# Performance work log

Hardware: AMD Instinct MI355X
Metric: run time of the kernel (lower is better)

Reference implementation:

```python
import jax, jax.numpy as jnp
import numpy as np

CODEBOOK_SIZE = 8192
EMBED_DIM = 512
COMMITMENT_COST = 0.25
B, N = 16, 2048


def setup_inputs() -> dict:
    key = jax.random.key(0)
    kz, kc = jax.random.split(key)
    z = jax.random.normal(kz, (B, N, EMBED_DIM), dtype=jnp.float32)
    # torch init: uniform(-1/K, 1/K)
    scale = 1.0 / CODEBOOK_SIZE
    codebook = jax.random.uniform(kc, (CODEBOOK_SIZE, EMBED_DIM), dtype=jnp.float32,
                                  minval=-scale, maxval=scale)
    return {"z": z, "codebook": codebook}


def reference(z, codebook):
    Bd, Nd, D = z.shape
    flat_z = z.reshape(-1, D)  # (B*N, D)
    # squared L2 distances via expansion: ||z||^2 + ||e||^2 - 2 z.e
    distances = (jnp.sum(flat_z * flat_z, axis=1, keepdims=True)
                 + jnp.sum(codebook * codebook, axis=1)
                 - 2.0 * flat_z @ codebook.T)  # (B*N, K)
    indices = jnp.argmin(distances, axis=1)  # (B*N,)
    quantized = codebook[indices].reshape(Bd, Nd, D)
    # mse_loss default reduction='mean'
    codebook_loss = jnp.mean((jax.lax.stop_gradient(quantized) - z) ** 2)
    commitment_loss = jnp.mean((quantized - jax.lax.stop_gradient(z)) ** 2)
    vq_loss = codebook_loss + COMMITMENT_COST * commitment_loss
    # straight-through estimator
    quantized = z + jax.lax.stop_gradient(quantized - z)
    return quantized, indices.reshape(Bd, Nd), vq_loss
```

## Files before the change

### kernel.cpp

```cpp
#include <hip/hip_runtime.h>

#define M_ROWS 32768
#define DIM    512
#define KCB    8192
#define BM     128
#define BN     128
#define NSLAB  128

typedef int    i32x4  __attribute__((ext_vector_type(4)));
typedef unsigned long long u64;

#define AS1(p) ((const __attribute__((address_space(1))) void*)(p))
#define AS3(p) ((__attribute__((address_space(3))) void*)(p))

__global__ void __launch_bounds__(256)
vq_fragpack_i8(const float* __restrict__ x, unsigned char* __restrict__ dst,
               float scale, int nthr) {
    int u = blockIdx.x * 256 + threadIdx.x;
    if (u >= nthr) return;
    int l  = u & 63;
    int g  = (u >> 6) & 7;
    int s  = (u >> 9) & 7;
    int rb = u >> 12;
    int row = rb * 128 + g * 16 + (l & 15);
    int k   = s * 64 + (l >> 4) * 16;
    const float* src = x + (size_t)row * DIM + k;
    int dw[4];
    #pragma unroll
    for (int d4 = 0; d4 < 4; ++d4) {
        float4 v = *(const float4*)(src + d4 * 4);
        int b0 = __float2int_rn(v.x * scale);
        int b1 = __float2int_rn(v.y * scale);
        int b2 = __float2int_rn(v.z * scale);
        int b3 = __float2int_rn(v.w * scale);
        dw[d4] = (b0 & 255) | ((b1 & 255) << 8) | ((b2 & 255) << 16)
               | ((b3 & 255) << 24);
    }
    i32x4 o = { dw[0], dw[1], dw[2], dw[3] };
    *(i32x4*)(dst + (size_t)u * 16) = o;
}

__global__ void __launch_bounds__(256) vq_rownorm(const float* __restrict__ z,
                                                  float* __restrict__ A) {
    int row  = blockIdx.x * 4 + (threadIdx.x >> 6);
    int lane = threadIdx.x & 63;
    const float* zr = z + (size_t)row * DIM;
    float4 a = *(const float4*)(zr + lane * 4);
    float4 b = *(const float4*)(zr + 256 + lane * 4);
    float s = a.x*a.x + a.y*a.y + a.z*a.z + a.w*a.w
            + b.x*b.x + b.y*b.y + b.z*b.z + b.w*b.w;
    #pragma unroll
    for (int off = 32; off > 0; off >>= 1) s += __shfl_down(s, off, 64);
    if (lane == 0) A[row] = s;
}

__global__ void __launch_bounds__(256, 4)
vq_gemm(const unsigned char* __restrict__ zf, const unsigned char* __restrict__ ef,
        const float* __restrict__ Anorm, u64* __restrict__ cand) {
    extern __shared__ char lds[];
    const int tid  = threadIdx.x;
    const int lane = tid & 63;
    const int wid  = tid >> 6;
    const int wm   = wid >> 1;
    const int wn   = wid & 1;
    const int rb   = (int)blockIdx.x >> 6;
    const int cbk  = (int)blockIdx.x & 63;
    const char* zsrc = (const char*)zf + ((size_t)rb  << 16);
    const char* esrc = (const char*)ef + ((size_t)cbk << 16);

    i32x4 acc[4][4];
    #pragma unroll
    for (int m = 0; m < 4; ++m)
        #pragma unroll
        for (int n = 0; n < 4; ++n) acc[m][n] = (i32x4)0;

#define STAGE(t) do {                                                         \
    char* dst_ = lds + (((t) & 1) << 14);                                     \
    _Pragma("unroll")                                                         \
    for (int j = 0; j < 4; ++j) {                                             \
        int n2 = (wid << 2) | j;                    \
        const char* src_ = (n2 < 8)                                           \
            ? zsrc + (((t) << 13) + (n2 << 10)) + (lane << 4)                 \
            : esrc + (((t) << 13) + ((n2 - 8) << 10)) + (lane << 4);          \
        __builtin_amdgcn_global_load_lds(AS1(src_), AS3(dst_ + (n2 << 10)), 16, 0, 0); \
    }                                                                         \
} while (0)

#define COMPUTE(t) do {                                                       \
    const char* bufA_ = lds + (((t) & 1) << 14);                              \
    const char* bufB_ = bufA_ + 8192;                                         \
    i32x4 af[4];                                                              \
    _Pragma("unroll")                                                         \
    for (int m = 0; m < 4; ++m)                                               \
        af[m] = *(const i32x4*)(bufA_ + (((wm << 2) | m) << 10) + (lane << 4)); \
    i32x4 b0 = *(const i32x4*)(bufB_ + (((wn << 2) | 0) << 10) + (lane << 4)); \
    i32x4 b1 = *(const i32x4*)(bufB_ + (((wn << 2) | 1) << 10) + (lane << 4)); \
    __builtin_amdgcn_s_setprio(1);                                            \
    _Pragma("unroll")                                                         \
    for (int m = 0; m < 4; ++m) {                                             \
        acc[m][0] = __builtin_amdgcn_mfma_i32_16x16x64_i8(af[m], b0, acc[m][0], 0, 0, 0); \
        acc[m][1] = __builtin_amdgcn_mfma_i32_16x16x64_i8(af[m], b1, acc[m][1], 0, 0, 0); \
    }                                                                         \
    __builtin_amdgcn_s_setprio(0);                                            \
    i32x4 b2 = *(const i32x4*)(bufB_ + (((wn << 2) | 2) << 10) + (lane << 4)); \
    i32x4 b3 = *(const i32x4*)(bufB_ + (((wn << 2) | 3) << 10) + (lane << 4)); \
    __builtin_amdgcn_s_setprio(1);                                            \
    _Pragma("unroll")                                                         \
    for (int m = 0; m < 4; ++m) {                                             \
        acc[m][2] = __builtin_amdgcn_mfma_i32_16x16x64_i8(af[m], b2, acc[m][2], 0, 0, 0); \
        acc[m][3] = __builtin_amdgcn_mfma_i32_16x16x64_i8(af[m], b3, acc[m][3], 0, 0, 0); \
    }                                                                         \
    __builtin_amdgcn_s_setprio(0);                                            \
} while (0)

#define STEP2(t) do {                                                         \
    STAGE((t) + 1);                                                           \
    COMPUTE(t);                                                               \
    __syncthreads();                                                          \
} while (0)

    STAGE(0);
    __syncthreads();
    STEP2(0); STEP2(1); STEP2(2); STEP2(3); STEP2(4); STEP2(5); STEP2(6);
    COMPUTE(7);
    __syncthreads();

    const float INV = 2.0f / (16.0f * 8192.0f * 127.0f);
    float* As = (float*)lds;
    if (tid < BM) As[tid] = Anorm[rb * BM + tid];
    __syncthreads();

    const unsigned colbase = (unsigned)((cbk << 7) + (wn << 6) + (lane & 15));
    #pragma unroll
    for (int m = 0; m < 4; ++m) {
        #pragma unroll
        for (int rg = 0; rg < 4; ++rg) {
            int row_l = (wm << 6) + (m << 4) + ((lane >> 4) << 2) + rg;
            float Arow = As[row_l];
            unsigned abase = __float_as_uint(Arow) - 8192u;
            unsigned k1 = 0xFFFFFFFFu, k2 = 0xFFFFFFFFu;
            #pragma unroll
            for (int nj = 0; nj < 4; ++nj) {
                float t = (float)acc[m][nj][rg] * INV;
                float d = Arow - t;
                unsigned io = __float_as_uint(d) - abase;
                io = io > 65535u ? 65535u : io;
                unsigned key = io * 65536u + (colbase + (unsigned)(nj << 4));
                unsigned mx = key > k1 ? key : k1;
                k1 = key < k1 ? key : k1;
                k2 = mx < k2 ? mx : k2;
            }
            #pragma unroll
            for (int mk = 1; mk < 16; mk <<= 1) {
                unsigned o1 = (unsigned)__shfl_xor((int)k1, mk);
                unsigned o2 = (unsigned)__shfl_xor((int)k2, mk);
                unsigned lo = k1 < o1 ? k1 : o1;
                unsigned hi = k1 < o1 ? o1 : k1;
                unsigned so = k2 < o2 ? k2 : o2;
                k1 = lo;
                k2 = hi < so ? hi : so;
            }
            if ((lane & 15) == 0) {
                size_t base = (size_t)(rb * BM + row_l) * (2 * NSLAB)
                            + (size_t)(((cbk << 1) | wn) << 1);
                cand[base]     = ((u64)(abase + (k1 >> 16)) << 32) | (u64)(k1 & 0xFFFFu);
                cand[base + 1] = ((u64)(abase + (k2 >> 16)) << 32) | (u64)(k2 & 0xFFFFu);
            }
        }
    }
}

__global__ void __launch_bounds__(256)
vq_refine_gather(const float* __restrict__ z, const float* __restrict__ cb,
                 const float* __restrict__ Anorm, const u64* __restrict__ cand,
                 float* __restrict__ outQ, float* __restrict__ outIdx,
                 double* __restrict__ lossRow) {
    __shared__ float zs[4][DIM];
    __shared__ int   sc[4][128];
    int w = threadIdx.x >> 6, lane = threadIdx.x & 63;
    int row = blockIdx.x * 4 + w;

    const float* zr = z + (size_t)row * DIM;
    *(float4*)&zs[w][lane * 4]       = *(const float4*)(zr + lane * 4);
    *(float4*)&zs[w][256 + lane * 4] = *(const float4*)(zr + 256 + lane * 4);

    const u64* cr = cand + (size_t)row * (2 * NSLAB);
    u64 c[4];
    #pragma unroll
    for (int k = 0; k < 4; ++k) c[k] = cr[lane * 4 + k];
    u64 mn = c[0];
    #pragma unroll
    for (int k = 1; k < 4; ++k) if (c[k] < mn) mn = c[k];
    #pragma unroll
    for (int m = 32; m > 0; m >>= 1) { u64 o = __shfl_xor(mn, m); if (o < mn) mn = o; }
    float minD = __uint_as_float((unsigned)(mn >> 32));
    float thr = minD + 2e-3f;
    u64 below = ((u64)1 << lane) - 1;
    int base = 0;
    #pragma unroll
    for (int k = 0; k < 4; ++k) {
        bool sk = __uint_as_float((unsigned)(c[k] >> 32)) <= thr;
        u64 mk = __ballot(sk);
        if (sk) {
            int slot = base + __popcll(mk & below);
            if (slot < 128) sc[w][slot] = (int)(unsigned)c[k];
        }
        base += __popcll(mk);
    }
    int ns = base < 128 ? base : 128;
    __syncthreads();

    float Arow = Anorm[row];
    float4 zv0 = *(const float4*)&zs[w][lane * 8];
    float4 zv1 = *(const float4*)&zs[w][lane * 8 + 4];
    u64 best = ~0ull;
    for (int j = 0; j < ns; ++j) {
        int col = sc[w][j];
        const float* e = cb + (size_t)col * DIM + lane * 8;
        float4 ev0 = *(const float4*)e;
        float4 ev1 = *(const float4*)(e + 4);
        float p = zv0.x * ev0.x;
        p = fmaf(zv0.y, ev0.y, p);
        p = fmaf(zv0.z, ev0.z, p);
        p = fmaf(zv0.w, ev0.w, p);
        p = fmaf(zv1.x, ev1.x, p);
        p = fmaf(zv1.y, ev1.y, p);
        p = fmaf(zv1.z, ev1.z, p);
        p = fmaf(zv1.w, ev1.w, p);
        #pragma unroll
        for (int off = 32; off > 0; off >>= 1) p += __shfl_xor(p, off);
        float d = Arow - 2.0f * p;
        u64 pk = ((u64)__float_as_uint(d) << 32) | (unsigned)col;
        if (pk < best) best = pk;
    }
    int bi = (int)(unsigned)best;

    const float* q = cb + (size_t)bi * DIM;
    float* o = outQ + (size_t)row * DIM;
    double ls = 0.0;
    #pragma unroll
    for (int j = 0; j < 2; ++j) {
        int off = j * 256 + lane * 4;
        float4 qv = *(const float4*)(q + off);
        float4 zv = *(const float4*)&zs[w][off];
        float t0 = qv.x - zv.x, t1 = qv.y - zv.y;
        float t2 = qv.z - zv.z, t3 = qv.w - zv.w;
        float4 ov = { zv.x + t0, zv.y + t1, zv.z + t2, zv.w + t3 };
        *(float4*)(o + off) = ov;
        ls += (double)t0 * t0 + (double)t1 * t1
            + (double)t2 * t2 + (double)t3 * t3;
    }
    #pragma unroll
    for (int off = 32; off > 0; off >>= 1) ls += __shfl_down(ls, off, 64);
    if (lane == 0) { lossRow[row] = ls; outIdx[row] = (float)bi; }
}

__global__ void __launch_bounds__(256)
vq_loss_final(const double* __restrict__ lossRow, float* __restrict__ outLoss) {
    __shared__ double sm[256];
    double s = 0.0;
    for (int i = threadIdx.x; i < M_ROWS; i += 256) s += lossRow[i];
    sm[threadIdx.x] = s;
    __syncthreads();
    for (int st = 128; st > 0; st >>= 1) {
        if (threadIdx.x < st) sm[threadIdx.x] += sm[threadIdx.x + st];
        __syncthreads();
    }
    if (threadIdx.x == 0)
        outLoss[0] = (float)(1.25 * sm[0] / (double)((size_t)M_ROWS * DIM));
}

extern "C" void kernel_launch(void* const* d_in, const int* in_sizes, int n_in,
                              void* d_out, int out_size, void* d_ws, size_t ws_size,
                              hipStream_t stream) {
    const float* z  = (const float*)d_in[0];
    const float* cb = (const float*)d_in[1];

    float* out     = (float*)d_out;
    float* outQ    = out;
    float* outIdx  = out + (size_t)M_ROWS * DIM;
    float* outLoss = out + (size_t)M_ROWS * DIM + M_ROWS;

    unsigned char* zfrag = (unsigned char*)d_out;

    char* ws = (char*)d_ws;
    float*  A       = (float*)ws;            ws += (size_t)M_ROWS * 4;
    double* lossRow = (double*)ws;           ws += (size_t)M_ROWS * 8;
    unsigned char* efrag = (unsigned char*)ws; ws += (size_t)KCB * DIM;
    u64*    cand    = (u64*)ws;

    int nthr_z = M_ROWS * DIM / 16;
    int nthr_e = KCB * DIM / 16;
    hipLaunchKernelGGL(vq_fragpack_i8, dim3(nthr_z / 256), dim3(256), 0, stream,
                       z, zfrag, 16.0f, nthr_z);
    hipLaunchKernelGGL(vq_fragpack_i8, dim3(nthr_e / 256), dim3(256), 0, stream,
                       cb, efrag, 8192.0f * 127.0f, nthr_e);
    hipLaunchKernelGGL(vq_rownorm, dim3(M_ROWS / 4), dim3(256), 0, stream, z, A);
    hipLaunchKernelGGL(vq_gemm, dim3((M_ROWS / BM) * (KCB / BN)), dim3(256),
                       32768, stream, zfrag, efrag, A, cand);
    hipLaunchKernelGGL(vq_refine_gather, dim3(M_ROWS / 4), dim3(256), 0, stream,
                       z, cb, A, cand, outQ, outIdx, lossRow);
    hipLaunchKernelGGL(vq_loss_final, dim3(1), dim3(256), 0, stream, lossRow, outLoss);
}
```

Measured before the change: 399.0 us.

## Fuse z int8 packing with row-norm and remap GEMM block order across XCDs

Merges the z int8 fragment-packing kernel and the row-norm kernel into one pass, so z (64 MB fp32) is read once instead of twice and one launch goes away. The fused kernel writes 8-byte pieces into the same fragment layout, which means narrower stores than the 16-byte stores used before. The GEMM block index is also permuted (bid0&7 * 2048 + bid0>>3) so each of the 8 XCDs handles a contiguous range of row blocks. The aim is better L2 reuse of the z and codebook fragments, at some cost in cross-XCD balance.

```diff
diff --git a/kernel.cpp b/kernel.cpp
--- a/kernel.cpp
+++ b/kernel.cpp
@@ -12,6 +12,42 @@
 
 #define AS1(p) ((const __attribute__((address_space(1))) void*)(p))
 #define AS3(p) ((__attribute__((address_space(3))) void*)(p))
+
+__global__ void __launch_bounds__(256)
+vq_packnorm_z(const float* __restrict__ z, unsigned char* __restrict__ dst,
+              float* __restrict__ A) {
+    int w = threadIdx.x >> 6, j = threadIdx.x & 63;
+    int row = blockIdx.x * 4 + w;
+    const float* zr = z + (size_t)row * DIM + j * 8;
+    float4 v0 = *(const float4*)zr;
+    float4 v1 = *(const float4*)(zr + 4);
+
+    float s = v0.x*v0.x + v0.y*v0.y + v0.z*v0.z + v0.w*v0.w
+            + v1.x*v1.x + v1.y*v1.y + v1.z*v1.z + v1.w*v1.w;
+    #pragma unroll
+    for (int off = 32; off > 0; off >>= 1) s += __shfl_down(s, off, 64);
+    if (j == 0) A[row] = s;
+
+    int b0 = __float2int_rn(v0.x * 16.0f);
+    int b1 = __float2int_rn(v0.y * 16.0f);
+    int b2 = __float2int_rn(v0.z * 16.0f);
+    int b3 = __float2int_rn(v0.w * 16.0f);
+    int b4 = __float2int_rn(v1.x * 16.0f);
+    int b5 = __float2int_rn(v1.y * 16.0f);
+    int b6 = __float2int_rn(v1.z * 16.0f);
+    int b7 = __float2int_rn(v1.w * 16.0f);
+    int2 p;
+    p.x = (b0 & 255) | ((b1 & 255) << 8) | ((b2 & 255) << 16) | ((b3 & 255) << 24);
+    p.y = (b4 & 255) | ((b5 & 255) << 8) | ((b6 & 255) << 16) | ((b7 & 255) << 24);
+
+    int rb  = row >> 7;
+    int g   = (row >> 4) & 7;
+    int sdx = j >> 3;
+    int lhi = (j >> 1) & 3;
+    int l   = (lhi << 4) | (row & 15);
+    int u   = (rb << 12) | (sdx << 9) | (g << 6) | l;
+    *(int2*)(dst + ((size_t)u << 4) + ((j & 1) << 3)) = p;
+}
 
 __global__ void __launch_bounds__(256)
 vq_fragpack_i8(const float* __restrict__ x, unsigned char* __restrict__ dst,
@@ -40,20 +76,6 @@
     *(i32x4*)(dst + (size_t)u * 16) = o;
 }
 
-__global__ void __launch_bounds__(256) vq_rownorm(const float* __restrict__ z,
-                                                  float* __restrict__ A) {
-    int row  = blockIdx.x * 4 + (threadIdx.x >> 6);
-    int lane = threadIdx.x & 63;
-    const float* zr = z + (size_t)row * DIM;
-    float4 a = *(const float4*)(zr + lane * 4);
-    float4 b = *(const float4*)(zr + 256 + lane * 4);
-    float s = a.x*a.x + a.y*a.y + a.z*a.z + a.w*a.w
-            + b.x*b.x + b.y*b.y + b.z*b.z + b.w*b.w;
-    #pragma unroll
-    for (int off = 32; off > 0; off >>= 1) s += __shfl_down(s, off, 64);
-    if (lane == 0) A[row] = s;
-}
-
 __global__ void __launch_bounds__(256, 4)
 vq_gemm(const unsigned char* __restrict__ zf, const unsigned char* __restrict__ ef,
         const float* __restrict__ Anorm, u64* __restrict__ cand) {
@@ -63,8 +85,10 @@
     const int wid  = tid >> 6;
     const int wm   = wid >> 1;
     const int wn   = wid & 1;
-    const int rb   = (int)blockIdx.x >> 6;
-    const int cbk  = (int)blockIdx.x & 63;
+    const int bid0 = (int)blockIdx.x;
+    const int bid  = (bid0 & 7) * 2048 + (bid0 >> 3);
+    const int rb   = bid >> 6;
+    const int cbk  = bid & 63;
     const char* zsrc = (const char*)zf + ((size_t)rb  << 16);
     const char* esrc = (const char*)ef + ((size_t)cbk << 16);
 
@@ -289,13 +313,11 @@
     unsigned char* efrag = (unsigned char*)ws; ws += (size_t)KCB * DIM;
     u64*    cand    = (u64*)ws;
 
-    int nthr_z = M_ROWS * DIM / 16;
     int nthr_e = KCB * DIM / 16;
-    hipLaunchKernelGGL(vq_fragpack_i8, dim3(nthr_z / 256), dim3(256), 0, stream,
-                       z, zfrag, 16.0f, nthr_z);
+    hipLaunchKernelGGL(vq_packnorm_z, dim3(M_ROWS / 4), dim3(256), 0, stream,
+                       z, zfrag, A);
     hipLaunchKernelGGL(vq_fragpack_i8, dim3(nthr_e / 256), dim3(256), 0, stream,
                        cb, efrag, 8192.0f * 127.0f, nthr_e);
-    hipLaunchKernelGGL(vq_rownorm, dim3(M_ROWS / 4), dim3(256), 0, stream, z, A);
     hipLaunchKernelGGL(vq_gemm, dim3((M_ROWS / BM) * (KCB / BN)), dim3(256),
                        32768, stream, zfrag, efrag, A, cand);
     hipLaunchKernelGGL(vq_refine_gather, dim3(M_ROWS / 4), dim3(256), 0, stream,
```

Result: faster. 368.5 us (-7.6%).
